# Kernel tuning notes

Hardware: AMD Instinct MI355X
Metric: run time of the kernel (lower is better)

Reference implementation:

```python
import jax, jax.numpy as jnp
import numpy as np

N_NODES = 50000
N_EDGES = 800000


def _spmm(edge_row, edge_col, edge_w, h):
    # sparse adj @ h via gather + segment-sum: adj[r,c] = edge_w
    msgs = edge_w[:, None] * h[edge_col]          # [E, D] gather
    return jax.ops.segment_sum(msgs, edge_row, num_segments=N_NODES)


def setup_inputs() -> dict:
    key = jax.random.key(0)
    ks = jax.random.split(key, 8)
    x = jax.random.normal(ks[0], (N_NODES, 256), dtype=jnp.float32)
    edge_row = jax.random.randint(ks[1], (N_EDGES,), 0, N_NODES, dtype=jnp.int32)
    edge_col = jax.random.randint(ks[2], (N_EDGES,), 0, N_NODES, dtype=jnp.int32)
    edge_w = jax.random.uniform(ks[3], (N_EDGES,), dtype=jnp.float32)
    W1 = jax.random.normal(ks[4], (256, 128), dtype=jnp.float32) * 0.06
    b1 = jnp.zeros((128,), dtype=jnp.float32)
    W2 = jax.random.normal(ks[5], (128, 32), dtype=jnp.float32) * 0.09
    b2 = jnp.zeros((32,), dtype=jnp.float32)
    return {"x": x, "edge_row": edge_row, "edge_col": edge_col,
            "edge_w": edge_w, "W1": W1, "b1": b1, "W2": W2, "b2": b2}


def reference(x, edge_row, edge_col, edge_w, W1, b1, W2, b2):
    # Layer 1: support = X @ W1 ; out = relu(A @ support + b1)
    # (dropout is identity in eval mode)
    h = jax.nn.relu(_spmm(edge_row, edge_col, edge_w, x @ W1) + b1)
    # Layer 2
    out = jax.nn.relu(_spmm(edge_row, edge_col, edge_w, h @ W2) + b2)
    return out
```

## Files before the change

kernel.cpp:

```cpp
#include <hip/hip_runtime.h>

#define N_NODES 50000
#define N_EDGES 800000
#define D0 256
#define D1 128
#define D2 32
#define CAP 48
#define NB 391
#define BCAP 3072
#define EB 8192
#define SC_BLOCKS 98
#define SW_BLOCKS 4
#define G1_BLOCKS 782
#define RG_BLOCKS 1563

typedef unsigned short u16;
typedef unsigned int   u32;
typedef unsigned long long u64;
typedef __attribute__((ext_vector_type(8))) short bf16x8;
typedef __attribute__((ext_vector_type(4))) float f32x4;

__device__ inline u32 bf16rne(float f) {
    union { float f; u32 u; } c; c.f = f;
    return (c.u + 0x7FFFu + ((c.u >> 16) & 1u)) >> 16;
}
__device__ inline float bfhi(u32 v) {
    union { u32 u; float f; } c; c.u = v & 0xFFFF0000u; return c.f;
}
__device__ inline float bflo(u32 v) {
    union { u32 u; float f; } c; c.u = v << 16; return c.f;
}

__global__ __launch_bounds__(1024) void scatter_kernel(const int* __restrict__ erow,
                                                       const int* __restrict__ ecol,
                                                       const float* __restrict__ ew,
                                                       u32* __restrict__ bcur,
                                                       u64* __restrict__ ebuf,
                                                       const float* __restrict__ W1,
                                                       u16* __restrict__ Bsw1,
                                                       const float* __restrict__ W2,
                                                       u16* __restrict__ Bsw2) {
    __shared__ u32 hist[NB];
    __shared__ u32 lbase[NB];
    const int tid = threadIdx.x;
    if (blockIdx.x < SC_BLOCKS) {
        if (tid < NB) hist[tid] = 0;
        __syncthreads();
        const int ebase = blockIdx.x * EB;
        #pragma unroll
        for (int k = 0; k < EB / 1024; ++k) {
            const int e = ebase + k * 1024 + tid;
            if (e < N_EDGES) atomicAdd(&hist[erow[e] >> 7], 1u);
        }
        __syncthreads();
        if (tid < NB) {
            const u32 h = hist[tid];
            lbase[tid] = h ? atomicAdd(&bcur[tid], h) : 0u;
            hist[tid] = 0;
        }
        __syncthreads();
        #pragma unroll
        for (int k = 0; k < EB / 1024; ++k) {
            const int e = ebase + k * 1024 + tid;
            if (e < N_EDGES) {
                const int r = erow[e];
                const int c = ecol[e];
                const float w = ew[e];
                const int b = r >> 7;
                const u32 lr = atomicAdd(&hist[b], 1u);
                const u32 pos = lbase[b] + lr;
                if (pos < BCAP)
                    ebuf[(size_t)b * BCAP + pos] =
                        (u64)(u32)c | ((u64)(u32)(r & 127) << 16) | ((u64)bf16rne(w) << 32);
            }
        }
    } else if (blockIdx.x < SC_BLOCKS + SW_BLOCKS) {
        const int id = (blockIdx.x - SC_BLOCKS) * 1024 + tid;
        const int lane = id & 63;
        const int t    = (id >> 6) & 7;
        const int ks   = id >> 9;
        const int n     = t * 16 + (lane & 15);
        const int kbase = ks * 32 + (lane >> 4) * 8;
        u32 v[8];
        #pragma unroll
        for (int j = 0; j < 8; ++j) v[j] = bf16rne(W1[(kbase + j) * D1 + n]);
        uint4 w;
        w.x = v[0] | (v[1] << 16);
        w.y = v[2] | (v[3] << 16);
        w.z = v[4] | (v[5] << 16);
        w.w = v[6] | (v[7] << 16);
        ((uint4*)Bsw1)[id] = w;
    } else if (tid < 512) {
        const int id = tid;
        const int lane = id & 63;
        const int t    = (id >> 6) & 1;
        const int ks   = id >> 7;
        const int n     = t * 16 + (lane & 15);
        const int kbase = ks * 32 + (lane >> 4) * 8;
        u32 v[8];
        #pragma unroll
        for (int j = 0; j < 8; ++j) v[j] = bf16rne(W2[(kbase + j) * D2 + n]);
        uint4 w;
        w.x = v[0] | (v[1] << 16);
        w.y = v[2] | (v[3] << 16);
        w.z = v[4] | (v[5] << 16);
        w.w = v[6] | (v[7] << 16);
        ((uint4*)Bsw2)[id] = w;
    }
}

__global__ __launch_bounds__(256) void gb_kernel(const float* __restrict__ x,
                                                 const u16* __restrict__ Bsw1,
                                                 u16* __restrict__ s1b,
                                                 const u32* __restrict__ bcur,
                                                 const u64* __restrict__ ebuf,
                                                 int* __restrict__ cnt,
                                                 u32* __restrict__ eg) {
    __shared__ u32 seg[128 * CAP];
    __shared__ u32 lcnt[128];
    const int bid = blockIdx.x;
    if (bid < NB) {
        const int b = bid;
        for (int i = threadIdx.x; i < 128; i += 256) lcnt[i] = 0;
        __syncthreads();
        int n = (int)bcur[b];
        if (n > BCAP) n = BCAP;
        const u64* ep = ebuf + (size_t)b * BCAP;
        for (int i = threadIdx.x; i < n; i += 256) {
            const u64 e = ep[i];
            const u32 c  = (u32)(e & 0xFFFFu);
            const u32 lr = (u32)((e >> 16) & 0x7Fu);
            const u32 w  = (u32)(e >> 32);
            const u32 p = atomicAdd(&lcnt[lr], 1u);
            if (p < CAP)
                seg[lr * CAP + p] = c | (w << 16);
        }
        __syncthreads();
        const int rows = min(128, N_NODES - b * 128);
        for (int i = threadIdx.x; i < rows; i += 256)
            cnt[b * 128 + i] = (int)min(lcnt[i], (u32)CAP);
        u32* dst = eg + (size_t)b * 128 * CAP;
        const int nvec = rows * (CAP / 4);
        for (int i = threadIdx.x; i < nvec; i += 256)
            ((uint4*)dst)[i] = ((const uint4*)seg)[i];
    } else {
        const int gb   = bid - NB;
        const int lane = threadIdx.x & 63;
        const int wave = threadIdx.x >> 6;
        const int rowbase = gb * 64 + wave * 16;
        const int m    = lane & 15;
        const int quad = lane >> 4;
        int arow = rowbase + m;
        if (arow >= N_NODES) arow = N_NODES - 1;
        const float* aptr = x + (size_t)arow * D0 + quad * 8;

        f32x4 acc[8];
        #pragma unroll
        for (int t = 0; t < 8; ++t) acc[t] = (f32x4){0.f, 0.f, 0.f, 0.f};

        #pragma unroll
        for (int ks = 0; ks < 8; ++ks) {
            const float4 f0 = *(const float4*)(aptr + ks * 32);
            const float4 f1 = *(const float4*)(aptr + ks * 32 + 4);
            bf16x8 a;
            a[0] = (short)bf16rne(f0.x); a[1] = (short)bf16rne(f0.y);
            a[2] = (short)bf16rne(f0.z); a[3] = (short)bf16rne(f0.w);
            a[4] = (short)bf16rne(f1.x); a[5] = (short)bf16rne(f1.y);
            a[6] = (short)bf16rne(f1.z); a[7] = (short)bf16rne(f1.w);
            const u16* bp = Bsw1 + ((size_t)(ks * 8) * 64 + lane) * 8;
            #pragma unroll
            for (int t = 0; t < 8; ++t) {
                const bf16x8 b = *(const bf16x8*)(bp + (size_t)t * 64 * 8);
                acc[t] = __builtin_amdgcn_mfma_f32_16x16x32_bf16(a, b, acc[t], 0, 0, 0);
            }
        }
        const int orow = rowbase + quad * 4;
        #pragma unroll
        for (int r = 0; r < 4; ++r) {
            const int row = orow + r;
            if (row < N_NODES) {
                u16* op = s1b + (size_t)row * D1 + m;
                #pragma unroll
                for (int t = 0; t < 8; ++t) op[t * 16] = (u16)bf16rne(acc[t][r]);
            }
        }
    }
}

__global__ __launch_bounds__(256) void spmm1_slice_kernel(const int* __restrict__ cnt,
                                                          const u32* __restrict__ eg,
                                                          const u16* __restrict__ src,
                                                          const float* __restrict__ b1,
                                                          u16* __restrict__ hb) {
    const int tx = threadIdx.x;
    const int s  = blockIdx.x & 7;
    const int rg = blockIdx.x >> 3;
    const int row = rg * 32 + threadIdx.y;
    if (row >= N_NODES) return;
    int len = cnt[row];
    if (len > CAP) len = CAP;
    const u32* ep = eg + (size_t)row * CAP;
    const u16* sp = src + s * 16;
    float ax0=0.f, ay0=0.f, ax1=0.f, ay1=0.f, ax2=0.f, ay2=0.f, ax3=0.f, ay3=0.f;
    int j = 0;
    for (; j + 7 < len; j += 8) {
        const uint4 e4a = *(const uint4*)(ep + j);
        const uint4 e4b = *(const uint4*)(ep + j + 4);
        const u32 v0 = ((const u32*)(sp + (size_t)(e4a.x & 0xFFFFu) * D1))[tx];
        const u32 v1 = ((const u32*)(sp + (size_t)(e4a.y & 0xFFFFu) * D1))[tx];
        const u32 v2 = ((const u32*)(sp + (size_t)(e4a.z & 0xFFFFu) * D1))[tx];
        const u32 v3 = ((const u32*)(sp + (size_t)(e4a.w & 0xFFFFu) * D1))[tx];
        const u32 v4 = ((const u32*)(sp + (size_t)(e4b.x & 0xFFFFu) * D1))[tx];
        const u32 v5 = ((const u32*)(sp + (size_t)(e4b.y & 0xFFFFu) * D1))[tx];
        const u32 v6 = ((const u32*)(sp + (size_t)(e4b.z & 0xFFFFu) * D1))[tx];
        const u32 v7 = ((const u32*)(sp + (size_t)(e4b.w & 0xFFFFu) * D1))[tx];
        const float w0 = bfhi(e4a.x), w1 = bfhi(e4a.y), w2 = bfhi(e4a.z), w3 = bfhi(e4a.w);
        const float w4 = bfhi(e4b.x), w5 = bfhi(e4b.y), w6 = bfhi(e4b.z), w7 = bfhi(e4b.w);
        ax0 += w0 * bflo(v0); ay0 += w0 * bfhi(v0);
        ax1 += w1 * bflo(v1); ay1 += w1 * bfhi(v1);
        ax2 += w2 * bflo(v2); ay2 += w2 * bfhi(v2);
        ax3 += w3 * bflo(v3); ay3 += w3 * bfhi(v3);
        ax0 += w4 * bflo(v4); ay0 += w4 * bfhi(v4);
        ax1 += w5 * bflo(v5); ay1 += w5 * bfhi(v5);
        ax2 += w6 * bflo(v6); ay2 += w6 * bfhi(v6);
        ax3 += w7 * bflo(v7); ay3 += w7 * bfhi(v7);
    }
    for (; j + 3 < len; j += 4) {
        const uint4 e4 = *(const uint4*)(ep + j);
        const u32 v0 = ((const u32*)(sp + (size_t)(e4.x & 0xFFFFu) * D1))[tx];
        const u32 v1 = ((const u32*)(sp + (size_t)(e4.y & 0xFFFFu) * D1))[tx];
        const u32 v2 = ((const u32*)(sp + (size_t)(e4.z & 0xFFFFu) * D1))[tx];
        const u32 v3 = ((const u32*)(sp + (size_t)(e4.w & 0xFFFFu) * D1))[tx];
        const float w0 = bfhi(e4.x), w1 = bfhi(e4.y), w2 = bfhi(e4.z), w3 = bfhi(e4.w);
        ax0 += w0 * bflo(v0); ay0 += w0 * bfhi(v0);
        ax1 += w1 * bflo(v1); ay1 += w1 * bfhi(v1);
        ax2 += w2 * bflo(v2); ay2 += w2 * bfhi(v2);
        ax3 += w3 * bflo(v3); ay3 += w3 * bfhi(v3);
    }
    for (; j < len; ++j) {
        const u32 e0 = ep[j];
        const u32 v0 = ((const u32*)(sp + (size_t)(e0 & 0xFFFFu) * D1))[tx];
        const float w0 = bfhi(e0);
        ax0 += w0 * bflo(v0); ay0 += w0 * bfhi(v0);
    }
    const float2 bv = ((const float2*)(b1 + s * 16))[tx];
    float vx = ax0 + ax1 + ax2 + ax3 + bv.x; vx = vx > 0.f ? vx : 0.f;
    float vy = ay0 + ay1 + ay2 + ay3 + bv.y; vy = vy > 0.f ? vy : 0.f;
    ((u32*)(hb + (size_t)row * D1 + s * 16))[tx] = bf16rne(vx) | (bf16rne(vy) << 16);
}

__global__ __launch_bounds__(256) void gemm2_mfma_kernel(const u16* __restrict__ hb,
                                                         const u16* __restrict__ Bsw2,
                                                         u16* __restrict__ s2b) {
    const int lane = threadIdx.x & 63;
    const int wave = threadIdx.x >> 6;
    const int rowbase = blockIdx.x * 64 + wave * 16;
    const int m    = lane & 15;
    const int quad = lane >> 4;
    int arow = rowbase + m;
    if (arow >= N_NODES) arow = N_NODES - 1;
    const u16* aptr = hb + (size_t)arow * D1 + quad * 8;

    f32x4 acc0 = (f32x4){0.f,0.f,0.f,0.f};
    f32x4 acc1 = (f32x4){0.f,0.f,0.f,0.f};

    #pragma unroll
    for (int ks = 0; ks < 4; ++ks) {
        const bf16x8 a = *(const bf16x8*)(aptr + ks * 32);
        const u16* bp = Bsw2 + ((size_t)(ks * 2) * 64 + lane) * 8;
        const bf16x8 b0 = *(const bf16x8*)(bp);
        const bf16x8 b1 = *(const bf16x8*)(bp + (size_t)64 * 8);
        acc0 = __builtin_amdgcn_mfma_f32_16x16x32_bf16(a, b0, acc0, 0, 0, 0);
        acc1 = __builtin_amdgcn_mfma_f32_16x16x32_bf16(a, b1, acc1, 0, 0, 0);
    }
    const int orow = rowbase + quad * 4;
    #pragma unroll
    for (int r = 0; r < 4; ++r) {
        const int row = orow + r;
        if (row < N_NODES) {
            u16* op = s2b + (size_t)row * D2 + m;
            op[0]  = (u16)bf16rne(acc0[r]);
            op[16] = (u16)bf16rne(acc1[r]);
        }
    }
}

__global__ __launch_bounds__(256) void spmm_csr32_kernel(const int* __restrict__ cnt,
                                                         const u32* __restrict__ eg,
                                                         const u16* __restrict__ src,
                                                         const float* __restrict__ bias,
                                                         float* __restrict__ out) {
    const int lane = threadIdx.x;
    const int row  = blockIdx.x * 16 + threadIdx.y;
    if (row >= N_NODES) return;
    int len = cnt[row];
    if (len > CAP) len = CAP;
    const u32* ep = eg + (size_t)row * CAP;
    float ax0=0.f, ay0=0.f, ax1=0.f, ay1=0.f, ax2=0.f, ay2=0.f, ax3=0.f, ay3=0.f;
    int j = 0;
    for (; j + 7 < len; j += 8) {
        const uint4 e4a = *(const uint4*)(ep + j);
        const uint4 e4b = *(const uint4*)(ep + j + 4);
        const u32 v0 = ((const u32*)(src + (size_t)(e4a.x & 0xFFFFu) * D2))[lane];
        const u32 v1 = ((const u32*)(src + (size_t)(e4a.y & 0xFFFFu) * D2))[lane];
        const u32 v2 = ((const u32*)(src + (size_t)(e4a.z & 0xFFFFu) * D2))[lane];
        const u32 v3 = ((const u32*)(src + (size_t)(e4a.w & 0xFFFFu) * D2))[lane];
        const u32 v4 = ((const u32*)(src + (size_t)(e4b.x & 0xFFFFu) * D2))[lane];
        const u32 v5 = ((const u32*)(src + (size_t)(e4b.y & 0xFFFFu) * D2))[lane];
        const u32 v6 = ((const u32*)(src + (size_t)(e4b.z & 0xFFFFu) * D2))[lane];
        const u32 v7 = ((const u32*)(src + (size_t)(e4b.w & 0xFFFFu) * D2))[lane];
        const float w0 = bfhi(e4a.x), w1 = bfhi(e4a.y), w2 = bfhi(e4a.z), w3 = bfhi(e4a.w);
        const float w4 = bfhi(e4b.x), w5 = bfhi(e4b.y), w6 = bfhi(e4b.z), w7 = bfhi(e4b.w);
        ax0 += w0 * bflo(v0); ay0 += w0 * bfhi(v0);
        ax1 += w1 * bflo(v1); ay1 += w1 * bfhi(v1);
        ax2 += w2 * bflo(v2); ay2 += w2 * bfhi(v2);
        ax3 += w3 * bflo(v3); ay3 += w3 * bfhi(v3);
        ax0 += w4 * bflo(v4); ay0 += w4 * bfhi(v4);
        ax1 += w5 * bflo(v5); ay1 += w5 * bfhi(v5);
        ax2 += w6 * bflo(v6); ay2 += w6 * bfhi(v6);
        ax3 += w7 * bflo(v7); ay3 += w7 * bfhi(v7);
    }
    for (; j + 3 < len; j += 4) {
        const uint4 e4 = *(const uint4*)(ep + j);
        const u32 v0 = ((const u32*)(src + (size_t)(e4.x & 0xFFFFu) * D2))[lane];
        const u32 v1 = ((const u32*)(src + (size_t)(e4.y & 0xFFFFu) * D2))[lane];
        const u32 v2 = ((const u32*)(src + (size_t)(e4.z & 0xFFFFu) * D2))[lane];
        const u32 v3 = ((const u32*)(src + (size_t)(e4.w & 0xFFFFu) * D2))[lane];
        const float w0 = bfhi(e4.x), w1 = bfhi(e4.y), w2 = bfhi(e4.z), w3 = bfhi(e4.w);
        ax0 += w0 * bflo(v0); ay0 += w0 * bfhi(v0);
        ax1 += w1 * bflo(v1); ay1 += w1 * bfhi(v1);
        ax2 += w2 * bflo(v2); ay2 += w2 * bfhi(v2);
        ax3 += w3 * bflo(v3); ay3 += w3 * bfhi(v3);
    }
    for (; j < len; ++j) {
        const u32 e0 = ep[j];
        const u32 v0 = ((const u32*)(src + (size_t)(e0 & 0xFFFFu) * D2))[lane];
        const float w0 = bfhi(e0);
        ax0 += w0 * bflo(v0); ay0 += w0 * bfhi(v0);
    }
    const float2 b2v = ((const float2*)bias)[lane];
    float vx = ax0 + ax1 + ax2 + ax3 + b2v.x; vx = vx > 0.f ? vx : 0.f;
    float vy = ay0 + ay1 + ay2 + ay3 + b2v.y; vy = vy > 0.f ? vy : 0.f;
    ((float2*)(out + (size_t)row * D2))[lane] = make_float2(vx, vy);
}

extern "C" void kernel_launch(void* const* d_in, const int* in_sizes, int n_in,
                              void* d_out, int out_size, void* d_ws, size_t ws_size,
                              hipStream_t stream) {
    const float* x    = (const float*)d_in[0];
    const int*   erow = (const int*)  d_in[1];
    const int*   ecol = (const int*)  d_in[2];
    const float* ew   = (const float*)d_in[3];
    const float* W1   = (const float*)d_in[4];
    const float* b1   = (const float*)d_in[5];
    const float* W2   = (const float*)d_in[6];
    const float* b2   = (const float*)d_in[7];
    float* out = (float*)d_out;

    int* cnt   = (int*)d_ws;
    u32* bcur  = (u32*)(cnt + N_NODES);
    u32* eg    = (u32*)(bcur + 512);
    u16* Bsw1  = (u16*)(eg + (size_t)N_NODES * CAP);
    u16* Bsw2  = Bsw1 + 8 * 8 * 64 * 8;
    u16* s1b   = Bsw2 + 4 * 2 * 64 * 8;
    u16* hb    = s1b + (size_t)N_NODES * D1;
    u16* s2b   = hb + (size_t)N_NODES * D1;
    u64* ebuf  = (u64*)(s2b + (size_t)N_NODES * D2);

    hipMemsetAsync(bcur, 0, 512 * sizeof(u32), stream);
    scatter_kernel<<<SC_BLOCKS + SW_BLOCKS + 1, 1024, 0, stream>>>(
        erow, ecol, ew, bcur, ebuf, W1, Bsw1, W2, Bsw2);
    gb_kernel<<<NB + G1_BLOCKS, 256, 0, stream>>>(x, Bsw1, s1b, bcur, ebuf, cnt, eg);
    spmm1_slice_kernel<<<RG_BLOCKS * 8, dim3(8, 32), 0, stream>>>(cnt, eg, s1b, b1, hb);
    gemm2_mfma_kernel<<<(N_NODES + 63) / 64, 256, 0, stream>>>(hb, Bsw2, s2b);
    spmm_csr32_kernel<<<(N_NODES + 15) / 16, dim3(16, 16), 0, stream>>>(cnt, eg, s2b, b2, out);
}
```

Before: 229.3 us.

## Store s1 as per-slice planes and use nontemporal loads/stores for streams

The layer-1 support matrix is now written as 8 separate planes of 16 columns each, so each slice block of the first SpMM gathers from a compact 1.6MB plane with 32-byte rows. The goal is better cache locality per slice instead of strided access across 256-byte rows. Edge-list reads and final output/h writes also become nontemporal so these streamed data do not evict the gathered feature rows. The GEMM1 epilogue now writes scattered 2-byte stores across planes, which may cost more store traffic.

Result: slower. 241.0 us (+5.1%).

```diff
diff --git a/kernel.cpp b/kernel.cpp
--- a/kernel.cpp
+++ b/kernel.cpp
@@ -13,6 +13,7 @@
 #define SW_BLOCKS 4
 #define G1_BLOCKS 782
 #define RG_BLOCKS 1563
+#define PL ((size_t)N_NODES * 16)
 
 typedef unsigned short u16;
 typedef unsigned int   u32;
@@ -29,6 +30,13 @@
 }
 __device__ inline float bflo(u32 v) {
     union { u32 u; float f; } c; c.u = v << 16; return c.f;
+}
+__device__ inline uint4 nt_load_u4(const u32* p) {
+    const u64* q = (const u64*)p;
+    const u64 a = __builtin_nontemporal_load(q);
+    const u64 b = __builtin_nontemporal_load(q + 1);
+    uint4 r; r.x = (u32)a; r.y = (u32)(a >> 32); r.z = (u32)b; r.w = (u32)(b >> 32);
+    return r;
 }
 
 __global__ __launch_bounds__(1024) void scatter_kernel(const int* __restrict__ erow,
@@ -127,7 +135,7 @@
         if (n > BCAP) n = BCAP;
         const u64* ep = ebuf + (size_t)b * BCAP;
         for (int i = threadIdx.x; i < n; i += 256) {
-            const u64 e = ep[i];
+            const u64 e = __builtin_nontemporal_load(ep + i);
             const u32 c  = (u32)(e & 0xFFFFu);
             const u32 lr = (u32)((e >> 16) & 0x7Fu);
             const u32 w  = (u32)(e >> 32);
@@ -179,9 +187,9 @@
         for (int r = 0; r < 4; ++r) {
             const int row = orow + r;
             if (row < N_NODES) {
-                u16* op = s1b + (size_t)row * D1 + m;
                 #pragma unroll
-                for (int t = 0; t < 8; ++t) op[t * 16] = (u16)bf16rne(acc[t][r]);
+                for (int t = 0; t < 8; ++t)
+                    s1b[(size_t)t * PL + (size_t)row * 16 + m] = (u16)bf16rne(acc[t][r]);
             }
         }
     }
@@ -200,20 +208,20 @@
     int len = cnt[row];
     if (len > CAP) len = CAP;
     const u32* ep = eg + (size_t)row * CAP;
-    const u16* sp = src + s * 16;
+    const u16* sp = src + (size_t)s * PL;
     float ax0=0.f, ay0=0.f, ax1=0.f, ay1=0.f, ax2=0.f, ay2=0.f, ax3=0.f, ay3=0.f;
     int j = 0;
     for (; j + 7 < len; j += 8) {
-        const uint4 e4a = *(const uint4*)(ep + j);
-        const uint4 e4b = *(const uint4*)(ep + j + 4);
-        const u32 v0 = ((const u32*)(sp + (size_t)(e4a.x & 0xFFFFu) * D1))[tx];
-        const u32 v1 = ((const u32*)(sp + (size_t)(e4a.y & 0xFFFFu) * D1))[tx];
-        const u32 v2 = ((const u32*)(sp + (size_t)(e4a.z & 0xFFFFu) * D1))[tx];
-        const u32 v3 = ((const u32*)(sp + (size_t)(e4a.w & 0xFFFFu) * D1))[tx];
-        const u32 v4 = ((const u32*)(sp + (size_t)(e4b.x & 0xFFFFu) * D1))[tx];
-        const u32 v5 = ((const u32*)(sp + (size_t)(e4b.y & 0xFFFFu) * D1))[tx];
-        const u32 v6 = ((const u32*)(sp + (size_t)(e4b.z & 0xFFFFu) * D1))[tx];
-        const u32 v7 = ((const u32*)(sp + (size_t)(e4b.w & 0xFFFFu) * D1))[tx];
+        const uint4 e4a = nt_load_u4(ep + j);
+        const uint4 e4b = nt_load_u4(ep + j + 4);
+        const u32 v0 = ((const u32*)(sp + (size_t)(e4a.x & 0xFFFFu) * 16))[tx];
+        const u32 v1 = ((const u32*)(sp + (size_t)(e4a.y & 0xFFFFu) * 16))[tx];
+        const u32 v2 = ((const u32*)(sp + (size_t)(e4a.z & 0xFFFFu) * 16))[tx];
+        const u32 v3 = ((const u32*)(sp + (size_t)(e4a.w & 0xFFFFu) * 16))[tx];
+        const u32 v4 = ((const u32*)(sp + (size_t)(e4b.x & 0xFFFFu) * 16))[tx];
+        const u32 v5 = ((const u32*)(sp + (size_t)(e4b.y & 0xFFFFu) * 16))[tx];
+        const u32 v6 = ((const u32*)(sp + (size_t)(e4b.z & 0xFFFFu) * 16))[tx];
+        const u32 v7 = ((const u32*)(sp + (size_t)(e4b.w & 0xFFFFu) * 16))[tx];
         const float w0 = bfhi(e4a.x), w1 = bfhi(e4a.y), w2 = bfhi(e4a.z), w3 = bfhi(e4a.w);
         const float w4 = bfhi(e4b.x), w5 = bfhi(e4b.y), w6 = bfhi(e4b.z), w7 = bfhi(e4b.w);
         ax0 += w0 * bflo(v0); ay0 += w0 * bfhi(v0);
@@ -226,11 +234,11 @@
         ax3 += w7 * bflo(v7); ay3 += w7 * bfhi(v7);
     }
     for (; j + 3 < len; j += 4) {
-        const uint4 e4 = *(const uint4*)(ep + j);
-        const u32 v0 = ((const u32*)(sp + (size_t)(e4.x & 0xFFFFu) * D1))[tx];
-        const u32 v1 = ((const u32*)(sp + (size_t)(e4.y & 0xFFFFu) * D1))[tx];
-        const u32 v2 = ((const u32*)(sp + (size_t)(e4.z & 0xFFFFu) * D1))[tx];
-        const u32 v3 = ((const u32*)(sp + (size_t)(e4.w & 0xFFFFu) * D1))[tx];
+        const uint4 e4 = nt_load_u4(ep + j);
+        const u32 v0 = ((const u32*)(sp + (size_t)(e4.x & 0xFFFFu) * 16))[tx];
+        const u32 v1 = ((const u32*)(sp + (size_t)(e4.y & 0xFFFFu) * 16))[tx];
+        const u32 v2 = ((const u32*)(sp + (size_t)(e4.z & 0xFFFFu) * 16))[tx];
+        const u32 v3 = ((const u32*)(sp + (size_t)(e4.w & 0xFFFFu) * 16))[tx];
         const float w0 = bfhi(e4.x), w1 = bfhi(e4.y), w2 = bfhi(e4.z), w3 = bfhi(e4.w);
         ax0 += w0 * bflo(v0); ay0 += w0 * bfhi(v0);
         ax1 += w1 * bflo(v1); ay1 += w1 * bfhi(v1);
@@ -238,15 +246,16 @@
         ax3 += w3 * bflo(v3); ay3 += w3 * bfhi(v3);
     }
     for (; j < len; ++j) {
-        const u32 e0 = ep[j];
-        const u32 v0 = ((const u32*)(sp + (size_t)(e0 & 0xFFFFu) * D1))[tx];
+        const u32 e0 = __builtin_nontemporal_load(ep + j);
+        const u32 v0 = ((const u32*)(sp + (size_t)(e0 & 0xFFFFu) * 16))[tx];
         const float w0 = bfhi(e0);
         ax0 += w0 * bflo(v0); ay0 += w0 * bfhi(v0);
     }
     const float2 bv = ((const float2*)(b1 + s * 16))[tx];
     float vx = ax0 + ax1 + ax2 + ax3 + bv.x; vx = vx > 0.f ? vx : 0.f;
     float vy = ay0 + ay1 + ay2 + ay3 + bv.y; vy = vy > 0.f ? vy : 0.f;
-    ((u32*)(hb + (size_t)row * D1 + s * 16))[tx] = bf16rne(vx) | (bf16rne(vy) << 16);
+    __builtin_nontemporal_store(bf16rne(vx) | (bf16rne(vy) << 16),
+                                (u32*)(hb + (size_t)row * D1 + s * 16) + tx);
 }
 
 __global__ __launch_bounds__(256) void gemm2_mfma_kernel(const u16* __restrict__ hb,
@@ -299,8 +308,8 @@
     float ax0=0.f, ay0=0.f, ax1=0.f, ay1=0.f, ax2=0.f, ay2=0.f, ax3=0.f, ay3=0.f;
     int j = 0;
     for (; j + 7 < len; j += 8) {
-        const uint4 e4a = *(const uint4*)(ep + j);
-        const uint4 e4b = *(const uint4*)(ep + j + 4);
+        const uint4 e4a = nt_load_u4(ep + j);
+        const uint4 e4b = nt_load_u4(ep + j + 4);
         const u32 v0 = ((const u32*)(src + (size_t)(e4a.x & 0xFFFFu) * D2))[lane];
         const u32 v1 = ((const u32*)(src + (size_t)(e4a.y & 0xFFFFu) * D2))[lane];
         const u32 v2 = ((const u32*)(src + (size_t)(e4a.z & 0xFFFFu) * D2))[lane];
@@ -321,7 +330,7 @@
         ax3 += w7 * bflo(v7); ay3 += w7 * bfhi(v7);
     }
     for (; j + 3 < len; j += 4) {
-        const uint4 e4 = *(const uint4*)(ep + j);
+        const uint4 e4 = nt_load_u4(ep + j);
         const u32 v0 = ((const u32*)(src + (size_t)(e4.x & 0xFFFFu) * D2))[lane];
         const u32 v1 = ((const u32*)(src + (size_t)(e4.y & 0xFFFFu) * D2))[lane];
         const u32 v2 = ((const u32*)(src + (size_t)(e4.z & 0xFFFFu) * D2))[lane];
@@ -333,7 +342,7 @@
         ax3 += w3 * bflo(v3); ay3 += w3 * bfhi(v3);
     }
     for (; j < len; ++j) {
-        const u32 e0 = ep[j];
+        const u32 e0 = __builtin_nontemporal_load(ep + j);
         const u32 v0 = ((const u32*)(src + (size_t)(e0 & 0xFFFFu) * D2))[lane];
         const float w0 = bfhi(e0);
         ax0 += w0 * bflo(v0); ay0 += w0 * bfhi(v0);
@@ -341,7 +350,8 @@
     const float2 b2v = ((const float2*)bias)[lane];
     float vx = ax0 + ax1 + ax2 + ax3 + b2v.x; vx = vx > 0.f ? vx : 0.f;
     float vy = ay0 + ay1 + ay2 + ay3 + b2v.y; vy = vy > 0.f ? vy : 0.f;
-    ((float2*)(out + (size_t)row * D2))[lane] = make_float2(vx, vy);
+    union { float2 f; u64 u; } o; o.f = make_float2(vx, vy);
+    __builtin_nontemporal_store(o.u, (u64*)(out + (size_t)row * D2) + lane);
 }
 
 extern "C" void kernel_launch(void* const* d_in, const int* in_sizes, int n_in,
@@ -363,7 +373,7 @@
     u16* Bsw1  = (u16*)(eg + (size_t)N_NODES * CAP);
     u16* Bsw2  = Bsw1 + 8 * 8 * 64 * 8;
     u16* s1b   = Bsw2 + 4 * 2 * 64 * 8;
-    u16* hb    = s1b + (size_t)N_NODES * D1;
+    u16* hb    = s1b + 8 * PL;
     u16* s2b   = hb + (size_t)N_NODES * D1;
     u64* ebuf  = (u64*)(s2b + (size_t)N_NODES * D2);
 
```
